# Kernel tuning notes

Hardware: AMD Instinct MI355X
Metric: run time of the kernel (lower is better)

Reference implementation:

```python
import jax, jax.numpy as jnp
import numpy as np

B, S, D, H = 2048, 200, 64, 4
H1, H2 = 64, 32
F = 4 * D


def _prelu(x, a):
    return jnp.where(x > 0, x, a * x)


def setup_inputs() -> dict:
    key = jax.random.key(0)
    ks = jax.random.split(key, 12)
    inp = {
        "query": jax.random.normal(ks[0], (B, D), dtype=jnp.float32),
        "keys": jax.random.normal(ks[1], (B, S, D), dtype=jnp.float32),
        "keys_mask": jax.random.randint(ks[2], (B, S), 0, 2, dtype=jnp.int32),
        # per-head MLP params (torch Linear equivalent, stored as [in,out])
        "W1": jax.random.normal(ks[3], (H, F, H1), dtype=jnp.float32) / np.sqrt(F),
        "b1": jnp.zeros((H, H1), dtype=jnp.float32),
        "a1": jnp.full((H,), 0.25, dtype=jnp.float32),  # PReLU weight
        "W2": jax.random.normal(ks[4], (H, H1, H2), dtype=jnp.float32) / np.sqrt(H1),
        "b2": jnp.zeros((H, H2), dtype=jnp.float32),
        "a2": jnp.full((H,), 0.25, dtype=jnp.float32),
        "W3": jax.random.normal(ks[5], (H, H2), dtype=jnp.float32) / np.sqrt(H2),
        "b3": jnp.zeros((H,), dtype=jnp.float32),
        # output projection
        "Wo": jax.random.normal(ks[6], (D, D), dtype=jnp.float32) / np.sqrt(D),
        "bo": jnp.zeros((D,), dtype=jnp.float32),
    }
    return inp


def reference(query, keys, keys_mask, W1, b1, a1, W2, b2, a2, W3, b3, Wo, bo):
    # rich attention features: [keys, q, keys*q, keys-q] -> [B,S,4D]
    q = jnp.broadcast_to(query[:, None, :], keys.shape)
    x = jnp.concatenate([keys, q, keys * q, keys - q], axis=-1)
    # all heads at once: tiny per-head MLP with PReLU
    h = jnp.einsum('bsf,hfk->bhsk', x, W1) + b1[None, :, None, :]   # [B,H,S,H1]
    h = _prelu(h, a1[None, :, None, None])
    h = jnp.einsum('bhsk,hkm->bhsm', h, W2) + b2[None, :, None, :]  # [B,H,S,H2]
    h = _prelu(h, a2[None, :, None, None])
    scores = jnp.einsum('bhsm,hm->bhs', h, W3) + b3[None, :, None]  # [B,H,S]
    # mask + softmax + NaN->0 (all-masked rows)
    valid = (keys_mask != 0)[:, None, :]
    scores = jnp.where(valid, scores, -jnp.inf)
    w = jax.nn.softmax(scores, axis=-1)
    w = jnp.where(jnp.isnan(w), jnp.zeros_like(w), w)
    # weighted sum over keys, mean over heads
    out_h = jnp.einsum('bhs,bsd->bhd', w, keys)  # [B,H,D]
    combined = out_h.mean(axis=1)                # [B,D]
    return combined @ Wo + bo
```

## Files before the change

kernel.cpp:

```cpp
#include <hip/hip_runtime.h>
#include <math.h>

constexpr int B  = 2048;
constexpr int S  = 200;
constexpr int D  = 64;
constexpr int H  = 4;
constexpr int H1 = 64;
constexpr int H2 = 32;
constexpr int F  = 256;

constexpr int PK = 72;

typedef short bf16x8 __attribute__((ext_vector_type(8)));
typedef float f32x4  __attribute__((ext_vector_type(4)));
typedef unsigned uint4v __attribute__((ext_vector_type(4)));

__device__ __forceinline__ unsigned cvtpk(float a, float b) {
    unsigned r;
    asm volatile("v_cvt_pk_bf16_f32 %0, %1, %2" : "=v"(r) : "v"(a), "v"(b));
    return r;
}
__device__ __forceinline__ float lo16f(unsigned w) { return __builtin_bit_cast(float, w << 16); }
__device__ __forceinline__ float hi16f(unsigned w) { return __builtin_bit_cast(float, w & 0xffff0000u); }

constexpr size_t OUTH_OFF = 0;
constexpr size_t SAD_OFF  = 2u * 1024 * 1024;
constexpr size_t SC_OFF   = SAD_OFF + 4 * 4096 * 4;
constexpr size_t SBD_OFF  = SC_OFF  + 4 * 4096 * 4;
constexpr size_t W2I_OFF  = SBD_OFF + 4 * 4096 * 4;

__global__ __launch_bounds__(256) void build_kernel(
    const float* __restrict__ W1, const float* __restrict__ W2,
    float* __restrict__ sad, float* __restrict__ sc, float* __restrict__ sbd,
    ushort* __restrict__ w2i)
{
    const int h = blockIdx.x;
    const int t = threadIdx.x;
    const float* w1h = W1 + (size_t)h * F * H1;

    #pragma unroll
    for (int half = 0; half < 2; ++half) {
        const int sl = half * 256 + t;
        const int f  = sl >> 6, l = sl & 63;
        const int mt = f & 3, kk = f >> 2;
        const int k  = 16 * mt + (l & 15);
        const int d0 = 32 * kk + ((l >> 4) << 3);
        float vs[8], vc[8], vb[8];
        #pragma unroll
        for (int j = 0; j < 8; ++j) {
            const int d = d0 + j;
            float A  = w1h[d * 64 + k];
            float Bv = w1h[(64 + d) * 64 + k];
            float C  = w1h[(128 + d) * 64 + k];
            float Dv = w1h[(192 + d) * 64 + k];
            vs[j] = A + Dv; vc[j] = C; vb[j] = Bv - Dv;
        }
        const size_t off = ((size_t)h * 512 + sl) * 8;
        *(f32x4*)&sad[off]     = *(f32x4*)&vs[0];
        *(f32x4*)&sad[off + 4] = *(f32x4*)&vs[4];
        *(f32x4*)&sc [off]     = *(f32x4*)&vc[0];
        *(f32x4*)&sc [off + 4] = *(f32x4*)&vc[4];
        *(f32x4*)&sbd[off]     = *(f32x4*)&vb[0];
        *(f32x4*)&sbd[off + 4] = *(f32x4*)&vb[4];
    }

    {
        const int f2 = t >> 6, l = t & 63;
        const int mt2 = f2 & 1, w = f2 >> 1;
        const int m = 16 * mt2 + (l & 15), k20 = 32 * w + ((l >> 4) << 3);
        const float* w2h = W2 + (size_t)h * H1 * H2;
        uint4v u = { cvtpk(w2h[(k20 + 0) * 32 + m], w2h[(k20 + 1) * 32 + m]),
                     cvtpk(w2h[(k20 + 2) * 32 + m], w2h[(k20 + 3) * 32 + m]),
                     cvtpk(w2h[(k20 + 4) * 32 + m], w2h[(k20 + 5) * 32 + m]),
                     cvtpk(w2h[(k20 + 6) * 32 + m], w2h[(k20 + 7) * 32 + m]) };
        *(uint4v*)&w2i[((size_t)h * 4 + f2) * 512 + l * 8] = u;
    }
}

__global__ __launch_bounds__(256, 3) void fused_b_kernel(
    const float* __restrict__ query, const float* __restrict__ keys,
    const int* __restrict__ mask,
    const float* __restrict__ sad, const float* __restrict__ sc,
    const float* __restrict__ sbd, const ushort* __restrict__ w2i,
    const float* __restrict__ b1, const float* __restrict__ a1,
    const float* __restrict__ b2, const float* __restrict__ a2,
    const float* __restrict__ W3, const float* __restrict__ b3,
    float* __restrict__ outh)
{
    __shared__ ushort sK[208 * PK];
    __shared__ ushort relay[4][16 * PK];
    __shared__ float  sSc[4][208];

    const int b    = blockIdx.x;
    const int t    = threadIdx.x;
    const int lane = t & 63;
    const int h    = t >> 6;
    const int g    = lane >> 4;
    const int ln16 = lane & 15;

    int mval[4];
    #pragma unroll
    for (int c = 0; c < 4; ++c) {
        int s = lane + 64 * c;
        mval[c] = (s < S) ? mask[(size_t)b * S + s] : 0;
    }

    {
        const float4* k4 = (const float4*)(keys + (size_t)b * S * D);
        for (int idx = t; idx < S * D / 4; idx += 256) {
            float4 v = k4[idx];
            int s = idx >> 4, dc = (idx & 15) * 4;
            *(uint2*)&sK[s * PK + dc] = make_uint2(cvtpk(v.x, v.y), cvtpk(v.z, v.w));
        }
        for (int i = t; i < 8 * PK / 2; i += 256)
            ((unsigned*)&sK[200 * PK])[i] = 0;
    }

    const float* qb = query + (size_t)b * D;
    bf16x8 wh[4][2];
    float qtp0 = 0.f, qtp1 = 0.f, qtp2 = 0.f, qtp3 = 0.f;
    #pragma unroll
    for (int kk = 0; kk < 2; ++kk) {
        const int d0 = 32 * kk + 8 * g;
        f32x4 q0 = *(const f32x4*)&qb[d0];
        f32x4 q1 = *(const f32x4*)&qb[d0 + 4];
        #pragma unroll
        for (int mt = 0; mt < 4; ++mt) {
            const int f = kk * 4 + mt;
            const size_t off = ((size_t)h * 512 + f * 64 + lane) * 8;
            f32x4 s0 = *(const f32x4*)&sad[off], s1 = *(const f32x4*)&sad[off + 4];
            f32x4 c0 = *(const f32x4*)&sc [off], c1 = *(const f32x4*)&sc [off + 4];
            f32x4 bd0 = *(const f32x4*)&sbd[off], bd1 = *(const f32x4*)&sbd[off + 4];
            float w0 = s0[0] + q0[0] * c0[0], w1 = s0[1] + q0[1] * c0[1];
            float w2 = s0[2] + q0[2] * c0[2], w3 = s0[3] + q0[3] * c0[3];
            float w4 = s1[0] + q1[0] * c1[0], w5 = s1[1] + q1[1] * c1[1];
            float w6 = s1[2] + q1[2] * c1[2], w7 = s1[3] + q1[3] * c1[3];
            uint4v u = { cvtpk(w0, w1), cvtpk(w2, w3), cvtpk(w4, w5), cvtpk(w6, w7) };
            wh[mt][kk] = __builtin_bit_cast(bf16x8, u);
            float d = q0[0]*bd0[0] + q0[1]*bd0[1] + q0[2]*bd0[2] + q0[3]*bd0[3]
                    + q1[0]*bd1[0] + q1[1]*bd1[1] + q1[2]*bd1[2] + q1[3]*bd1[3];
            if (mt == 0) qtp0 += d; else if (mt == 1) qtp1 += d;
            else if (mt == 2) qtp2 += d; else qtp3 += d;
        }
    }
    qtp0 += __shfl_xor(qtp0, 16); qtp0 += __shfl_xor(qtp0, 32);
    qtp1 += __shfl_xor(qtp1, 16); qtp1 += __shfl_xor(qtp1, 32);
    qtp2 += __shfl_xor(qtp2, 16); qtp2 += __shfl_xor(qtp2, 32);
    qtp3 += __shfl_xor(qtp3, 16); qtp3 += __shfl_xor(qtp3, 32);
    f32x4 qtv[4];
    #pragma unroll
    for (int mt = 0; mt < 4; ++mt) {
        float src = (mt == 0) ? qtp0 : (mt == 1) ? qtp1 : (mt == 2) ? qtp2 : qtp3;
        f32x4 b1v = *(const f32x4*)&b1[h * 64 + mt * 16 + 4 * g];
        f32x4 v;
        #pragma unroll
        for (int i = 0; i < 4; ++i) v[i] = __shfl(src, 4 * g + i) + b1v[i];
        qtv[mt] = v;
    }

    bf16x8 w2f[2][2];
    #pragma unroll
    for (int w = 0; w < 2; ++w)
        #pragma unroll
        for (int mt2 = 0; mt2 < 2; ++mt2)
            w2f[w][mt2] = *(const bf16x8*)&w2i[((size_t)h * 4 + w * 2 + mt2) * 512 + lane * 8];
    f32x4 b2v[2], w3v[2];
    #pragma unroll
    for (int mt2 = 0; mt2 < 2; ++mt2) {
        b2v[mt2] = *(const f32x4*)&b2[h * 32 + mt2 * 16 + 4 * g];
        w3v[mt2] = *(const f32x4*)&W3[h * 32 + mt2 * 16 + 4 * g];
    }
    const float a1v = a1[h], a2v = a2[h], b3v = b3[h];

    __syncthreads();

    ushort* myR = relay[h];

    for (int st = 0; st < 13; ++st) {
        bf16x8 bk0 = *(const bf16x8*)&sK[(st * 16 + ln16) * PK + 0  + 8 * g];
        bf16x8 bk1 = *(const bf16x8*)&sK[(st * 16 + ln16) * PK + 32 + 8 * g];

        f32x4 acc[4] = { qtv[0], qtv[1], qtv[2], qtv[3] };
        #pragma unroll
        for (int mt = 0; mt < 4; ++mt)
            acc[mt] = __builtin_amdgcn_mfma_f32_16x16x32_bf16(wh[mt][0], bk0, acc[mt], 0, 0, 0);
        #pragma unroll
        for (int mt = 0; mt < 4; ++mt)
            acc[mt] = __builtin_amdgcn_mfma_f32_16x16x32_bf16(wh[mt][1], bk1, acc[mt], 0, 0, 0);

        #pragma unroll
        for (int mt = 0; mt < 4; ++mt) {
            float v0 = acc[mt][0]; v0 = v0 > 0.f ? v0 : a1v * v0;
            float v1 = acc[mt][1]; v1 = v1 > 0.f ? v1 : a1v * v1;
            float v2 = acc[mt][2]; v2 = v2 > 0.f ? v2 : a1v * v2;
            float v3 = acc[mt][3]; v3 = v3 > 0.f ? v3 : a1v * v3;
            *(uint2*)&myR[ln16 * PK + mt * 16 + 4 * g] =
                make_uint2(cvtpk(v0, v1), cvtpk(v2, v3));
        }

        f32x4 acc2[2] = { b2v[0], b2v[1] };
        #pragma unroll
        for (int w = 0; w < 2; ++w) {
            bf16x8 Bh = *(const bf16x8*)&myR[ln16 * PK + w * 32 + 8 * g];
            #pragma unroll
            for (int mt2 = 0; mt2 < 2; ++mt2)
                acc2[mt2] = __builtin_amdgcn_mfma_f32_16x16x32_bf16(w2f[w][mt2], Bh, acc2[mt2], 0, 0, 0);
        }

        float part = 0.f;
        #pragma unroll
        for (int mt2 = 0; mt2 < 2; ++mt2) {
            #pragma unroll
            for (int i = 0; i < 4; ++i) {
                float v = acc2[mt2][i];
                v = v > 0.f ? v : a2v * v;
                part += v * w3v[mt2][i];
            }
        }
        part += __shfl_xor(part, 16);
        part += __shfl_xor(part, 32);
        const int s = st * 16 + ln16;
        if (lane < 16 && s < 200) sSc[h][s] = part + b3v;
    }

    {
        float v[4];
        float M = -INFINITY;
        #pragma unroll
        for (int c = 0; c < 4; ++c) {
            int s = lane + 64 * c;
            v[c] = (s < S && mval[c]) ? sSc[h][s] : -INFINITY;
            M = fmaxf(M, v[c]);
        }
        #pragma unroll
        for (int off = 32; off > 0; off >>= 1) M = fmaxf(M, __shfl_xor(M, off));
        float Z = 0.f, e[4];
        #pragma unroll
        for (int c = 0; c < 4; ++c) { e[c] = mval[c] ? __expf(v[c] - M) : 0.f; Z += e[c]; }
        #pragma unroll
        for (int off = 32; off > 0; off >>= 1) Z += __shfl_xor(Z, off);
        const float inv = Z > 0.f ? 1.f / Z : 0.f;
        #pragma unroll
        for (int c = 0; c < 4; ++c) { int s = lane + 64 * c; if (s < S) sSc[h][s] = e[c] * inv; }
    }

    {
        const int sg = lane >> 4, dq = ln16;
        float ax = 0.f, ay = 0.f, az = 0.f, aw = 0.f;
        #pragma unroll 5
        for (int i = 0; i < 50; ++i) {
            const int s = sg * 50 + i;
            const float w = sSc[h][s];
            uint2 kv = *(const uint2*)&sK[s * PK + 4 * dq];
            ax += w * lo16f(kv.x); ay += w * hi16f(kv.x);
            az += w * lo16f(kv.y); aw += w * hi16f(kv.y);
        }
        ax += __shfl_xor(ax, 16); ay += __shfl_xor(ay, 16);
        az += __shfl_xor(az, 16); aw += __shfl_xor(aw, 16);
        ax += __shfl_xor(ax, 32); ay += __shfl_xor(ay, 32);
        az += __shfl_xor(az, 32); aw += __shfl_xor(aw, 32);
        if (lane < 16) {
            float4 o = { ax, ay, az, aw };
            *(float4*)&outh[((size_t)b * H + h) * D + 4 * dq] = o;
        }
    }
}

__global__ __launch_bounds__(256) void proj_kernel(
    const float* __restrict__ outh, const float* __restrict__ Wo,
    const float* __restrict__ bo, float* __restrict__ out)
{
    __shared__ float comb[4][64];
    const int t = threadIdx.x, bb = t >> 6, j = t & 63;
    const size_t b = (size_t)blockIdx.x * 4 + bb;

    const float* oh = outh + b * H * D;
    comb[bb][j] = 0.25f * (oh[j] + oh[64 + j] + oh[128 + j] + oh[192 + j]);
    __syncthreads();

    float o = bo[j];
    #pragma unroll 8
    for (int d = 0; d < 64; ++d)
        o += comb[bb][d] * Wo[d * 64 + j];
    out[b * D + j] = o;
}

extern "C" void kernel_launch(void* const* d_in, const int* in_sizes, int n_in,
                              void* d_out, int out_size, void* d_ws, size_t ws_size,
                              hipStream_t stream) {
    const float* query = (const float*)d_in[0];
    const float* keys  = (const float*)d_in[1];
    const int*   mask  = (const int*)d_in[2];
    const float* W1 = (const float*)d_in[3];
    const float* b1 = (const float*)d_in[4];
    const float* a1 = (const float*)d_in[5];
    const float* W2 = (const float*)d_in[6];
    const float* b2 = (const float*)d_in[7];
    const float* a2 = (const float*)d_in[8];
    const float* W3 = (const float*)d_in[9];
    const float* b3 = (const float*)d_in[10];
    const float* Wo = (const float*)d_in[11];
    const float* bo = (const float*)d_in[12];

    float* out  = (float*)d_out;
    char*  ws   = (char*)d_ws;
    float* outh = (float*)(ws + OUTH_OFF);
    float* sad  = (float*)(ws + SAD_OFF);
    float* sc   = (float*)(ws + SC_OFF);
    float* sbd  = (float*)(ws + SBD_OFF);
    ushort* w2i = (ushort*)(ws + W2I_OFF);

    build_kernel<<<dim3(H), 256, 0, stream>>>(W1, W2, sad, sc, sbd, w2i);
    fused_b_kernel<<<dim3(B), 256, 0, stream>>>(
        query, keys, mask, sad, sc, sbd, w2i, b1, a1, b2, a2, W3, b3, outh);
    proj_kernel<<<dim3(B / 4), 256, 0, stream>>>(outh, Wo, bo, out);
}
```

Baseline: 69.90 us.

## Fuse output projection into attention kernel and keep scores in registers

Folds the head-mean and Wo projection into the main per-batch kernel, removing the proj kernel launch and the outh round trip through global memory. Scores stay in registers per tile, with the mask packed into a per-lane bitmask, so the shared-memory score array goes away and the relay buffer is reused as scratch. Shared memory drops and launch bounds rise to 4 blocks per CU. The cost is extra register pressure and two more block barriers, plus Wo reads from every block.

```diff
diff --git a/kernel.cpp b/kernel.cpp
--- a/kernel.cpp
+++ b/kernel.cpp
@@ -23,11 +23,10 @@
 __device__ __forceinline__ float lo16f(unsigned w) { return __builtin_bit_cast(float, w << 16); }
 __device__ __forceinline__ float hi16f(unsigned w) { return __builtin_bit_cast(float, w & 0xffff0000u); }
 
-constexpr size_t OUTH_OFF = 0;
-constexpr size_t SAD_OFF  = 2u * 1024 * 1024;
-constexpr size_t SC_OFF   = SAD_OFF + 4 * 4096 * 4;
-constexpr size_t SBD_OFF  = SC_OFF  + 4 * 4096 * 4;
-constexpr size_t W2I_OFF  = SBD_OFF + 4 * 4096 * 4;
+constexpr size_t SAD_OFF = 0;
+constexpr size_t SC_OFF  = SAD_OFF + 4 * 4096 * 4;
+constexpr size_t SBD_OFF = SC_OFF  + 4 * 4096 * 4;
+constexpr size_t W2I_OFF = SBD_OFF + 4 * 4096 * 4;
 
 __global__ __launch_bounds__(256) void build_kernel(
     const float* __restrict__ W1, const float* __restrict__ W2,
@@ -77,7 +76,7 @@
     }
 }
 
-__global__ __launch_bounds__(256, 3) void fused_b_kernel(
+__global__ __launch_bounds__(256, 4) void fused_b_kernel(
     const float* __restrict__ query, const float* __restrict__ keys,
     const int* __restrict__ mask,
     const float* __restrict__ sad, const float* __restrict__ sc,
@@ -85,11 +84,11 @@
     const float* __restrict__ b1, const float* __restrict__ a1,
     const float* __restrict__ b2, const float* __restrict__ a2,
     const float* __restrict__ W3, const float* __restrict__ b3,
-    float* __restrict__ outh)
+    const float* __restrict__ Wo, const float* __restrict__ bo,
+    float* __restrict__ out)
 {
-    __shared__ ushort sK[208 * PK];
+    __shared__ ushort sK[200 * PK];
     __shared__ ushort relay[4][16 * PK];
-    __shared__ float  sSc[4][208];
 
     const int b    = blockIdx.x;
     const int t    = threadIdx.x;
@@ -98,11 +97,23 @@
     const int g    = lane >> 4;
     const int ln16 = lane & 15;
 
-    int mval[4];
-    #pragma unroll
-    for (int c = 0; c < 4; ++c) {
-        int s = lane + 64 * c;
-        mval[c] = (s < S) ? mask[(size_t)b * S + s] : 0;
+    unsigned mbits = 0;
+    {
+        int mval[4];
+        #pragma unroll
+        for (int c = 0; c < 4; ++c) {
+            int s = lane + 64 * c;
+            mval[c] = (s < S) ? mask[(size_t)b * S + s] : 0;
+        }
+        #pragma unroll
+        for (int st = 0; st < 13; ++st) {
+            const int src = 16 * (st & 3) + ln16;
+            int v = (st >> 2) == 0 ? __shfl(mval[0], src)
+                  : (st >> 2) == 1 ? __shfl(mval[1], src)
+                  : (st >> 2) == 2 ? __shfl(mval[2], src)
+                  :                  __shfl(mval[3], src);
+            mbits |= (v != 0) ? (1u << st) : 0u;
+        }
     }
 
     {
@@ -112,8 +123,6 @@
             int s = idx >> 4, dc = (idx & 15) * 4;
             *(uint2*)&sK[s * PK + dc] = make_uint2(cvtpk(v.x, v.y), cvtpk(v.z, v.w));
         }
-        for (int i = t; i < 8 * PK / 2; i += 256)
-            ((unsigned*)&sK[200 * PK])[i] = 0;
     }
 
     const float* qb = query + (size_t)b * D;
@@ -175,10 +184,14 @@
     __syncthreads();
 
     ushort* myR = relay[h];
-
+    float sc13[13];
+
+    #pragma unroll
     for (int st = 0; st < 13; ++st) {
-        bf16x8 bk0 = *(const bf16x8*)&sK[(st * 16 + ln16) * PK + 0  + 8 * g];
-        bf16x8 bk1 = *(const bf16x8*)&sK[(st * 16 + ln16) * PK + 32 + 8 * g];
+        int srow = st * 16 + ln16;
+        srow = srow > 199 ? 199 : srow;
+        bf16x8 bk0 = *(const bf16x8*)&sK[srow * PK + 0  + 8 * g];
+        bf16x8 bk1 = *(const bf16x8*)&sK[srow * PK + 32 + 8 * g];
 
         f32x4 acc[4] = { qtv[0], qtv[1], qtv[2], qtv[3] };
         #pragma unroll
@@ -219,29 +232,33 @@
         }
         part += __shfl_xor(part, 16);
         part += __shfl_xor(part, 32);
-        const int s = st * 16 + ln16;
-        if (lane < 16 && s < 200) sSc[h][s] = part + b3v;
-    }
-
-    {
-        float v[4];
+        sc13[st] = part + b3v;
+    }
+
+    float* ws = (float*)myR;
+    {
         float M = -INFINITY;
         #pragma unroll
-        for (int c = 0; c < 4; ++c) {
-            int s = lane + 64 * c;
-            v[c] = (s < S && mval[c]) ? sSc[h][s] : -INFINITY;
-            M = fmaxf(M, v[c]);
-        }
-        #pragma unroll
-        for (int off = 32; off > 0; off >>= 1) M = fmaxf(M, __shfl_xor(M, off));
-        float Z = 0.f, e[4];
-        #pragma unroll
-        for (int c = 0; c < 4; ++c) { e[c] = mval[c] ? __expf(v[c] - M) : 0.f; Z += e[c]; }
-        #pragma unroll
-        for (int off = 32; off > 0; off >>= 1) Z += __shfl_xor(Z, off);
+        for (int st = 0; st < 13; ++st)
+            if ((mbits >> st) & 1) M = fmaxf(M, sc13[st]);
+        #pragma unroll
+        for (int off = 1; off < 16; off <<= 1) M = fmaxf(M, __shfl_xor(M, off));
+        float Z = 0.f, e[13];
+        #pragma unroll
+        for (int st = 0; st < 13; ++st) {
+            e[st] = ((mbits >> st) & 1) ? __expf(sc13[st] - M) : 0.f;
+            Z += e[st];
+        }
+        #pragma unroll
+        for (int off = 1; off < 16; off <<= 1) Z += __shfl_xor(Z, off);
         const float inv = Z > 0.f ? 1.f / Z : 0.f;
-        #pragma unroll
-        for (int c = 0; c < 4; ++c) { int s = lane + 64 * c; if (s < S) sSc[h][s] = e[c] * inv; }
+        if (g == 0) {
+            #pragma unroll
+            for (int st = 0; st < 13; ++st) {
+                const int s = st * 16 + ln16;
+                if (st < 12 || ln16 < 8) ws[s] = e[st] * inv;
+            }
+        }
     }
 
     {
@@ -250,7 +267,7 @@
         #pragma unroll 5
         for (int i = 0; i < 50; ++i) {
             const int s = sg * 50 + i;
-            const float w = sSc[h][s];
+            const float w = ws[s];
             uint2 kv = *(const uint2*)&sK[s * PK + 4 * dq];
             ax += w * lo16f(kv.x); ay += w * hi16f(kv.x);
             az += w * lo16f(kv.y); aw += w * hi16f(kv.y);
@@ -261,28 +278,32 @@
         az += __shfl_xor(az, 32); aw += __shfl_xor(aw, 32);
         if (lane < 16) {
             float4 o = { ax, ay, az, aw };
-            *(float4*)&outh[((size_t)b * H + h) * D + 4 * dq] = o;
-        }
-    }
-}
-
-__global__ __launch_bounds__(256) void proj_kernel(
-    const float* __restrict__ outh, const float* __restrict__ Wo,
-    const float* __restrict__ bo, float* __restrict__ out)
-{
-    __shared__ float comb[4][64];
-    const int t = threadIdx.x, bb = t >> 6, j = t & 63;
-    const size_t b = (size_t)blockIdx.x * 4 + bb;
-
-    const float* oh = outh + b * H * D;
-    comb[bb][j] = 0.25f * (oh[j] + oh[64 + j] + oh[128 + j] + oh[192 + j]);
+            *(float4*)&ws[200 + 4 * dq] = o;
+        }
+    }
     __syncthreads();
 
-    float o = bo[j];
-    #pragma unroll 8
-    for (int d = 0; d < 64; ++d)
-        o += comb[bb][d] * Wo[d * 64 + j];
-    out[b * D + j] = o;
+    {
+        float p = 0.f;
+        #pragma unroll
+        for (int j = 0; j < 16; ++j) {
+            const int d = 16 * h + j;
+            const float cmb = 0.25f * (((const float*)relay[0])[200 + d]
+                                     + ((const float*)relay[1])[200 + d]
+                                     + ((const float*)relay[2])[200 + d]
+                                     + ((const float*)relay[3])[200 + d]);
+            p += cmb * Wo[d * 64 + lane];
+        }
+        ws[264 + lane] = p;
+    }
+    __syncthreads();
+    if (t < 64) {
+        float o = bo[t] + ((const float*)relay[0])[264 + t]
+                        + ((const float*)relay[1])[264 + t]
+                        + ((const float*)relay[2])[264 + t]
+                        + ((const float*)relay[3])[264 + t];
+        out[(size_t)b * D + t] = o;
+    }
 }
 
 extern "C" void kernel_launch(void* const* d_in, const int* in_sizes, int n_in,
@@ -304,7 +325,6 @@
 
     float* out  = (float*)d_out;
     char*  ws   = (char*)d_ws;
-    float* outh = (float*)(ws + OUTH_OFF);
     float* sad  = (float*)(ws + SAD_OFF);
     float* sc   = (float*)(ws + SC_OFF);
     float* sbd  = (float*)(ws + SBD_OFF);
@@ -312,6 +332,6 @@
 
     build_kernel<<<dim3(H), 256, 0, stream>>>(W1, W2, sad, sc, sbd, w2i);
     fused_b_kernel<<<dim3(B), 256, 0, stream>>>(
-        query, keys, mask, sad, sc, sbd, w2i, b1, a1, b2, a2, W3, b3, outh);
-    proj_kernel<<<dim3(B / 4), 256, 0, stream>>>(outh, Wo, bo, out);
+        query, keys, mask, sad, sc, sbd, w2i, b1, a1, b2, a2, W3, b3,
+        Wo, bo, out);
 }
```

Result: faster. 66.27 us (-5.2%).
